# Optimization experiments

Measured on AMD Instinct MI355X. Metric: run time of the kernel, lower is better.

## Reference

```python
import jax, jax.numpy as jnp
import numpy as np
from jax import lax

B, H, S = 256, 256, 512


def setup_inputs() -> dict:
    key = jax.random.key(0)
    ks = jax.random.split(key, 7)
    sc = 1.0 / np.sqrt(H).astype(np.float32)
    tree_state = jax.random.normal(ks[0], (B, H), jnp.float32)
    seq_states = jax.random.normal(ks[1], (B, H, S), jnp.float32)
    seq_mask = jax.random.randint(ks[2], (B, S), 0, 2, jnp.int32)
    W_ih = jax.random.uniform(ks[3], (3 * H, H), jnp.float32, -sc, sc)
    W_hh = jax.random.uniform(ks[4], (3 * H, H), jnp.float32, -sc, sc)
    b_ih = jax.random.uniform(ks[5], (3 * H,), jnp.float32, -sc, sc)
    b_hh = jax.random.uniform(ks[6], (3 * H,), jnp.float32, -sc, sc)
    return {"tree_state": tree_state, "seq_states": seq_states, "seq_mask": seq_mask,
            "W_ih": W_ih, "W_hh": W_hh, "b_ih": b_ih, "b_hh": b_hh}


def _gru_cell(x, h, W_ih, W_hh, b_ih, b_hh):
    # torch.nn.GRUCell math. x, h: (B, H); W_*: (3H, H); b_*: (3H,)
    gi = x @ W_ih.T + b_ih          # (B, 3H)
    gh = h @ W_hh.T + b_hh          # (B, 3H)
    i_r, i_z, i_n = jnp.split(gi, 3, axis=-1)
    h_r, h_z, h_n = jnp.split(gh, 3, axis=-1)
    r = jax.nn.sigmoid(i_r + h_r)
    z = jax.nn.sigmoid(i_z + h_z)
    n = jnp.tanh(i_n + r * h_n)
    return (1.0 - z) * n + z * h


def reference(tree_state, seq_states, seq_mask, W_ih, W_hh, b_ih, b_hh):
    # sequential recurrent scan over the seq axis of seq_states (batch, hid, seq)
    xs = jnp.transpose(seq_states, (2, 0, 1))  # (S, B, H)

    def step(h, x):
        h_new = _gru_cell(x, h, W_ih, W_hh, b_ih, b_hh)
        return h_new, h_new

    _, outs = lax.scan(step, tree_state, xs)      # (S, B, H)
    rnn_out = jnp.transpose(outs, (1, 0, 2))      # (B, S, H)
    # get_final_encoder_states: last unmasked timestep per row
    last_idx = jnp.maximum(jnp.sum(seq_mask, axis=1) - 1, 0)  # (B,)
    final = jnp.take_along_axis(rnn_out, last_idx[:, None, None], axis=1)  # (B,1,H)
    return final[:, 0, :]
```

## Files before the change

kernel.cpp:

```cpp
#include <hip/hip_runtime.h>
#include <hip/hip_bf16.h>

#define HH 256
#define SSL 512
#define G3 768

using short8 = __attribute__((ext_vector_type(8))) short;
using f32x4  = __attribute__((ext_vector_type(4))) float;

__device__ __forceinline__ unsigned short f2bf(float f) {
  unsigned int u = __float_as_uint(f);
  u += 0x7FFFu + ((u >> 16) & 1u);
  return (unsigned short)(u >> 16);
}
__device__ __forceinline__ float bf2f(unsigned short b) {
  return __uint_as_float(((unsigned int)b) << 16);
}
__device__ __forceinline__ void block_sync_lds() {
  asm volatile("s_waitcnt lgkmcnt(0)\n\ts_barrier" ::: "memory");
}

__global__ __launch_bounds__(256) void prep_pack(
    const float* __restrict__ Wih, const float* __restrict__ Whh,
    unsigned short* __restrict__ wih_bf, unsigned short* __restrict__ whh_frag)
{
  int blk = blockIdx.x;
  if (blk < 96) {
    int base = (blk * 256 + threadIdx.x) * 4;
#pragma unroll
    for (int i = 0; i < 4; i++) {
      int u = base + i;
      float a = Wih[2 * u], b = Wih[2 * u + 1];
      ((unsigned int*)wih_bf)[u] = (unsigned int)f2bf(a) | ((unsigned int)f2bf(b) << 16);
    }
  } else {
    int gid = (blk - 96) * 256 + threadIdx.x;
    int f = gid >> 6, l = gid & 63;
    int kt = f & 7, mt = (f >> 3) & 1, g = (f >> 4) % 3, w = f / 48;
    int row = g * HH + w * 32 + mt * 16 + (l & 15);
    int k0  = kt * 32 + (l >> 4) * 8;
    const float* src = Whh + (size_t)row * HH + k0;
    unsigned int o[4];
#pragma unroll
    for (int i = 0; i < 4; i++)
      o[i] = (unsigned int)f2bf(src[2 * i]) | ((unsigned int)f2bf(src[2 * i + 1]) << 16);
    *(uint4*)(whh_frag + ((size_t)f * 64 + l) * 8) = *(uint4*)o;
  }
}

__global__ __launch_bounds__(512, 4) void gi_gemm(
    const float* __restrict__ X, const unsigned short* __restrict__ Wb,
    const float* __restrict__ bih, const float* __restrict__ bhh,
    unsigned short* __restrict__ gi)
{
  __shared__ __align__(16) char smem[36864];
  unsigned short* Al = (unsigned short*)smem;
  unsigned short* Bl = (unsigned short*)(smem + 16384);
  float (*Dl)[132] = (float(*)[132])smem;

  const int tid  = threadIdx.x;
  const int lane = tid & 63;
  const int wave = tid >> 6;
  const int wm   = wave >> 2;
  const int wj   = wave & 3;
  const int n16  = lane & 15;
  const int quad = lane >> 4;

  const int mblk = blockIdx.y;
  const int b    = mblk >> 2;
  const int s0   = (mblk & 3) * 128;
  const int j0   = blockIdx.x * 128;

  f32x4 acc[4][2];
#pragma unroll
  for (int mt = 0; mt < 4; mt++)
#pragma unroll
    for (int jt = 0; jt < 2; jt++) acc[mt][jt] = f32x4{0.f, 0.f, 0.f, 0.f};

  const float* Xb = X + (size_t)b * (HH * SSL);

  float4 xa[2][2];
  uint4  wbv[2];

  auto ldA = [&](int kt, int q, float4* dst) {
    int idx = tid + 512 * q, sq = idx & 31, a = idx >> 5;
    const float* p = Xb + (size_t)(kt * 64 + 2 * a) * SSL + s0 + 4 * sq;
    dst[0] = *(const float4*)p;
    dst[1] = *(const float4*)(p + SSL);
  };
  auto ldB = [&](int kt, int q) -> uint4 {
    int cid = tid + 512 * q, j = cid >> 3, c = cid & 7;
    return *(const uint4*)(Wb + (size_t)(j0 + j) * HH + kt * 64 + c * 8);
  };

  ldA(0, 0, xa[0]); ldA(0, 1, xa[1]);
  wbv[0] = ldB(0, 0); wbv[1] = ldB(0, 1);

  for (int kt = 0; kt < 4; kt++) {
#pragma unroll
    for (int q = 0; q < 2; q++) {
      int idx = tid + 512 * q, sq = idx & 31, a = idx >> 5;
      int c = a >> 2, d = a & 3;
#pragma unroll
      for (int r = 0; r < 4; r++) {
        int s = 4 * sq + r;
        int sw = (s + (s >> 3)) & 7;
        unsigned int u =
            (unsigned int)f2bf(((const float*)&xa[q][0])[r]) |
            ((unsigned int)f2bf(((const float*)&xa[q][1])[r]) << 16);
        *(unsigned int*)(Al + s * 64 + ((c ^ sw) * 8) + d * 2) = u;
      }
    }
#pragma unroll
    for (int p = 0; p < 2; p++) {
      int cid = tid + 512 * p, j = cid >> 3, c = cid & 7;
      int sw = (j + (j >> 3)) & 7;
      *(uint4*)(Bl + j * 64 + ((c ^ sw) * 8)) = wbv[p];
    }
    __syncthreads();
    if (kt < 3) {
      ldA(kt + 1, 0, xa[0]); ldA(kt + 1, 1, xa[1]);
      wbv[0] = ldB(kt + 1, 0); wbv[1] = ldB(kt + 1, 1);
    }
#pragma unroll
    for (int kk = 0; kk < 2; kk++) {
      short8 af[4], bfr[2];
#pragma unroll
      for (int mt = 0; mt < 4; mt++) {
        int s = wm * 64 + mt * 16 + n16;
        int sw = (s + (s >> 3)) & 7;
        af[mt] = *(const short8*)(Al + s * 64 + (((kk * 4 + quad) ^ sw) * 8));
      }
#pragma unroll
      for (int jt = 0; jt < 2; jt++) {
        int j = wj * 32 + jt * 16 + n16;
        int sw = (j + (j >> 3)) & 7;
        bfr[jt] = *(const short8*)(Bl + j * 64 + (((kk * 4 + quad) ^ sw) * 8));
      }
#pragma unroll
      for (int mt = 0; mt < 4; mt++)
#pragma unroll
        for (int jt = 0; jt < 2; jt++)
          acc[mt][jt] = __builtin_amdgcn_mfma_f32_16x16x32_bf16(af[mt], bfr[jt], acc[mt][jt], 0, 0, 0);
    }
    __syncthreads();
  }

  float bias[2];
  {
    int jg0 = j0 + wj * 32 + 0 * 16 + n16;
    int jg1 = j0 + wj * 32 + 1 * 16 + n16;
    bias[0] = bih[jg0] + (jg0 < 2 * HH ? bhh[jg0] : 0.f);
    bias[1] = bih[jg1] + (jg1 < 2 * HH ? bhh[jg1] : 0.f);
  }

  for (int c = 0; c < 2; c++) {
    __syncthreads();
    if (wm == c) {
#pragma unroll
      for (int mt = 0; mt < 4; mt++)
#pragma unroll
        for (int jt = 0; jt < 2; jt++)
#pragma unroll
          for (int r = 0; r < 4; r++)
            Dl[mt * 16 + quad * 4 + r][wj * 32 + jt * 16 + n16] = acc[mt][jt][r] + bias[jt];
    }
    __syncthreads();
#pragma unroll
    for (int i = 0; i < 2; i++) {
      int ml = (tid >> 4) + 32 * i;
      int jj = (tid & 15) * 8;
      float4 p0 = *(const float4*)&Dl[ml][jj];
      float4 p1 = *(const float4*)&Dl[ml][jj + 4];
      short8 st;
      st[0] = (short)f2bf(p0.x); st[1] = (short)f2bf(p0.y);
      st[2] = (short)f2bf(p0.z); st[3] = (short)f2bf(p0.w);
      st[4] = (short)f2bf(p1.x); st[5] = (short)f2bf(p1.y);
      st[6] = (short)f2bf(p1.z); st[7] = (short)f2bf(p1.w);
      int sgl = s0 + c * 64 + ml;
      *(short8*)(gi + ((size_t)b * SSL + sgl) * G3 + j0 + jj) = st;
    }
  }
}

__global__ __launch_bounds__(512, 2) void gru_scan(
    const float* __restrict__ tree, const int* __restrict__ mask,
    const unsigned short* __restrict__ wfrag, const float* __restrict__ bhh,
    const unsigned short* __restrict__ gi, float* __restrict__ out)
{
  __shared__ __align__(16) unsigned char lds[82432];
  unsigned short* wlds = (unsigned short*)lds;
  unsigned short (*hfrag)[8][4][4][8] =
      (unsigned short(*)[8][4][4][8])(lds + 65536);
  float* preF = (float*)(lds + 69632);
  int*   lsum = (int*)(lds + 82304);

  const int tid  = threadIdx.x;
  const int lane = tid & 63;
  const int w    = tid >> 6;
  const int n16  = lane & 15;
  const int quad = lane >> 4;
  const int brow0 = blockIdx.x * 4;
  const int bb = tid >> 7;
  const int jj = (tid & 127) * 2;

  if (tid < 4) lsum[tid] = 0;
#pragma unroll
  for (int i = 0; i < 8; i++) {
    int cid = tid + 512 * i;
    int l = cid & 63, rest = cid >> 6;
    int ktp = rest & 3, mtp = (rest >> 2) & 1, wp = rest >> 3;
    int F = ((wp * 3 + 2) * 2 + mtp) * 8 + (4 + ktp);
    uint4 v = *(const uint4*)(wfrag + ((size_t)F * 64 + l) * 8);
    *(uint4*)(wlds + (((size_t)((wp * 2 + mtp) * 4 + ktp)) * 64 + l) * 8) = v;
  }
  __syncthreads();
  {
    const int* mp = mask + (size_t)(brow0 + bb) * SSL + (tid & 127) * 4;
    atomicAdd(&lsum[bb], mp[0] + mp[1] + mp[2] + mp[3]);
  }

  short8 aw[2][2][8];
#pragma unroll
  for (int g = 0; g < 2; g++)
#pragma unroll
    for (int mt = 0; mt < 2; mt++)
#pragma unroll
      for (int kt = 0; kt < 8; kt++) {
        int F = ((w * 3 + g) * 2 + mt) * 8 + kt;
        aw[g][mt][kt] = *(const short8*)(wfrag + ((size_t)F * 64 + lane) * 8);
      }
  short8 awC[2][4];
#pragma unroll
  for (int mt = 0; mt < 2; mt++)
#pragma unroll
    for (int kt = 0; kt < 4; kt++) {
      int F = ((w * 3 + 2) * 2 + mt) * 8 + kt;
      awC[mt][kt] = *(const short8*)(wfrag + ((size_t)F * 64 + lane) * 8);
    }
#pragma unroll
  for (int g = 0; g < 2; g++)
#pragma unroll
    for (int mt = 0; mt < 2; mt++)
#pragma unroll
      for (int kt = 0; kt < 8; kt++)
        asm volatile("" : "+a"(aw[g][mt][kt]));
#pragma unroll
  for (int mt = 0; mt < 2; mt++)
#pragma unroll
    for (int kt = 0; kt < 4; kt++)
      asm volatile("" : "+a"(awC[mt][kt]));

  float bhn0 = bhh[2 * HH + jj], bhn1 = bhh[2 * HH + jj + 1];

  float h0 = tree[(size_t)(brow0 + bb) * HH + jj];
  float h1 = tree[(size_t)(brow0 + bb) * HH + jj + 1];
  *(unsigned int*)&hfrag[0][jj >> 5][bb][(jj >> 3) & 3][jj & 7] =
      (unsigned int)f2bf(h0) | ((unsigned int)f2bf(h1) << 16);
  __syncthreads();
  int last = lsum[bb] - 1; if (last < 0) last = 0;

  const unsigned short* gib = gi + (size_t)(brow0 + bb) * SSL * G3;
  unsigned int giA[3], giB[3];
#pragma unroll
  for (int g = 0; g < 3; g++) giA[g] = *(const unsigned int*)(gib + (size_t)0 * G3 + g * HH + jj);
#pragma unroll
  for (int g = 0; g < 3; g++) giB[g] = *(const unsigned int*)(gib + (size_t)1 * G3 + g * HH + jj);

  auto step = [&](int t, unsigned int* gv) {
    const int cb = t & 1, nb = cb ^ 1;
    float gir0 = bf2f((unsigned short)(gv[0] & 0xFFFF)), gir1 = bf2f((unsigned short)(gv[0] >> 16));
    float giz0 = bf2f((unsigned short)(gv[1] & 0xFFFF)), giz1 = bf2f((unsigned short)(gv[1] >> 16));
    float gin0 = bf2f((unsigned short)(gv[2] & 0xFFFF)), gin1 = bf2f((unsigned short)(gv[2] >> 16));

#pragma unroll
    for (int mt = 0; mt < 2; mt++) {
      f32x4 a0 = f32x4{0.f, 0.f, 0.f, 0.f};
      f32x4 a1 = f32x4{0.f, 0.f, 0.f, 0.f};
      f32x4 a2 = f32x4{0.f, 0.f, 0.f, 0.f};
#pragma unroll
      for (int kt = 0; kt < 8; kt++) {
        short8 hb = *(const short8*)&hfrag[cb][kt][n16 & 3][quad][0];
        a0 = __builtin_amdgcn_mfma_f32_16x16x32_bf16(aw[0][mt][kt], hb, a0, 0, 0, 0);
        a1 = __builtin_amdgcn_mfma_f32_16x16x32_bf16(aw[1][mt][kt], hb, a1, 0, 0, 0);
        short8 w2 = (kt < 4) ? awC[mt][kt]
                  : *(const short8*)(wlds + (((size_t)((w * 2 + mt) * 4 + (kt - 4))) * 64 + lane) * 8);
        a2 = __builtin_amdgcn_mfma_f32_16x16x32_bf16(w2, hb, a2, 0, 0, 0);
      }
      if (n16 < 4) {
        *(f32x4*)(preF + 0 * 1056 + n16 * 264 + w * 32 + mt * 16 + quad * 4) = a0;
        *(f32x4*)(preF + 1 * 1056 + n16 * 264 + w * 32 + mt * 16 + quad * 4) = a1;
        *(f32x4*)(preF + 2 * 1056 + n16 * 264 + w * 32 + mt * 16 + quad * 4) = a2;
      }
    }
    int tn = (t + 2 < SSL) ? t + 2 : SSL - 1;
    gv[0] = *(const unsigned int*)(gib + (size_t)tn * G3 + 0 * HH + jj);
    gv[1] = *(const unsigned int*)(gib + (size_t)tn * G3 + 1 * HH + jj);
    gv[2] = *(const unsigned int*)(gib + (size_t)tn * G3 + 2 * HH + jj);
    block_sync_lds();

    float2 pr = *(const float2*)(preF + 0 * 1056 + bb * 264 + jj);
    float2 pz = *(const float2*)(preF + 1 * 1056 + bb * 264 + jj);
    float2 pn = *(const float2*)(preF + 2 * 1056 + bb * 264 + jj);
    float hr0 = pr.x + gir0, hr1 = pr.y + gir1;
    float hz0 = pz.x + giz0, hz1 = pz.y + giz1;
    float hn0 = pn.x + bhn0, hn1 = pn.y + bhn1;
    float r0 = __builtin_amdgcn_rcpf(1.f + __expf(-hr0));
    float r1 = __builtin_amdgcn_rcpf(1.f + __expf(-hr1));
    float z0 = __builtin_amdgcn_rcpf(1.f + __expf(-hz0));
    float z1 = __builtin_amdgcn_rcpf(1.f + __expf(-hz1));
    float a0 = gin0 + r0 * hn0, a1 = gin1 + r1 * hn1;
    float nn0 = 1.f - 2.f * __builtin_amdgcn_rcpf(__expf(2.f * a0) + 1.f);
    float nn1 = 1.f - 2.f * __builtin_amdgcn_rcpf(__expf(2.f * a1) + 1.f);
    float hN0 = nn0 + z0 * (h0 - nn0);
    float hN1 = nn1 + z1 * (h1 - nn1);
    h0 = hN0; h1 = hN1;
    *(unsigned int*)&hfrag[nb][jj >> 5][bb][(jj >> 3) & 3][jj & 7] =
        (unsigned int)f2bf(hN0) | ((unsigned int)f2bf(hN1) << 16);
    if (t == last) {
      out[(size_t)(brow0 + bb) * HH + jj] = hN0;
      out[(size_t)(brow0 + bb) * HH + jj + 1] = hN1;
    }
    block_sync_lds();
  };

  for (int t = 0; t < SSL; t += 2) {
    step(t, giA);
    step(t + 1, giB);
  }
}

extern "C" void kernel_launch(void* const* d_in, const int* in_sizes, int n_in,
                              void* d_out, int out_size, void* d_ws, size_t ws_size,
                              hipStream_t stream) {
  const float* tree = (const float*)d_in[0];
  const float* seq  = (const float*)d_in[1];
  const int*   mask = (const int*)d_in[2];
  const float* Wih  = (const float*)d_in[3];
  const float* Whh  = (const float*)d_in[4];
  const float* bih  = (const float*)d_in[5];
  const float* bhh  = (const float*)d_in[6];
  float* out = (float*)d_out;

  unsigned short* gi      = (unsigned short*)d_ws;
  unsigned short* wih_bf  = (unsigned short*)((char*)d_ws + 201326592);
  unsigned short* whh_frag= (unsigned short*)((char*)d_ws + 201719808);

  prep_pack<<<192, 256, 0, stream>>>(Wih, Whh, wih_bf, whh_frag);
  gi_gemm<<<dim3(6, 1024), 512, 0, stream>>>(seq, wih_bf, bih, bhh, gi);
  gru_scan<<<64, 512, 0, stream>>>(tree, mask, whh_frag, bhh, gi, out);
}
```

Measured before the change: 1.007 ms.

## Halve scan block to 4 waves, keep all W_hh fragments in registers

The recurrent scan kernel moves from 8 waves to 4 waves per block, each wave owning 64 gate rows. The whole W_hh slice now lives in AGPRs and VGPRs instead of partly in LDS. The h-state buffer gets a padded layout, and each thread handles 4 hidden elements with wider gi loads. The aim is to cut per-step LDS weight traffic and barrier cost across fewer waves, in exchange for more MFMAs per wave and heavy register pressure at one block per CU.

```diff
diff --git a/kernel.cpp b/kernel.cpp
--- a/kernel.cpp
+++ b/kernel.cpp
@@ -36,8 +36,8 @@
   } else {
     int gid = (blk - 96) * 256 + threadIdx.x;
     int f = gid >> 6, l = gid & 63;
-    int kt = f & 7, mt = (f >> 3) & 1, g = (f >> 4) % 3, w = f / 48;
-    int row = g * HH + w * 32 + mt * 16 + (l & 15);
+    int kt = f & 7, mt = (f >> 3) & 3, g = (f >> 5) % 3, w = f / 96;
+    int row = g * HH + w * 64 + mt * 16 + (l & 15);
     int k0  = kt * 32 + (l >> 4) * 8;
     const float* src = Whh + (size_t)row * HH + k0;
     unsigned int o[4];
@@ -183,17 +183,14 @@
   }
 }
 
-__global__ __launch_bounds__(512, 2) void gru_scan(
+__global__ __launch_bounds__(256, 1) void gru_scan(
     const float* __restrict__ tree, const int* __restrict__ mask,
     const unsigned short* __restrict__ wfrag, const float* __restrict__ bhh,
     const unsigned short* __restrict__ gi, float* __restrict__ out)
 {
-  __shared__ __align__(16) unsigned char lds[82432];
-  unsigned short* wlds = (unsigned short*)lds;
-  unsigned short (*hfrag)[8][4][4][8] =
-      (unsigned short(*)[8][4][4][8])(lds + 65536);
-  float* preF = (float*)(lds + 69632);
-  int*   lsum = (int*)(lds + 82304);
+  __shared__ __align__(16) unsigned short hbuf[2][1088];
+  __shared__ __align__(16) float preF[3][4][264];
+  __shared__ int lsum[4];
 
   const int tid  = threadIdx.x;
   const int lane = tid & 63;
@@ -201,132 +198,145 @@
   const int n16  = lane & 15;
   const int quad = lane >> 4;
   const int brow0 = blockIdx.x * 4;
-  const int bb = tid >> 7;
-  const int jj = (tid & 127) * 2;
+  const int jj   = lane * 4;
 
   if (tid < 4) lsum[tid] = 0;
-#pragma unroll
-  for (int i = 0; i < 8; i++) {
-    int cid = tid + 512 * i;
-    int l = cid & 63, rest = cid >> 6;
-    int ktp = rest & 3, mtp = (rest >> 2) & 1, wp = rest >> 3;
-    int F = ((wp * 3 + 2) * 2 + mtp) * 8 + (4 + ktp);
-    uint4 v = *(const uint4*)(wfrag + ((size_t)F * 64 + l) * 8);
-    *(uint4*)(wlds + (((size_t)((wp * 2 + mtp) * 4 + ktp)) * 64 + l) * 8) = v;
+
+  f32x4 h4 = *(const f32x4*)(tree + (size_t)(brow0 + w) * HH + jj);
+  float h0 = h4[0], h1 = h4[1], h2 = h4[2], h3 = h4[3];
+  const int wslot = ((jj >> 5) * 17 + w * 4 + ((jj >> 3) & 3)) * 8 + (jj & 7);
+  {
+    unsigned long long u =
+        (unsigned long long)((unsigned)f2bf(h0) | ((unsigned)f2bf(h1) << 16)) |
+        ((unsigned long long)((unsigned)f2bf(h2) | ((unsigned)f2bf(h3) << 16)) << 32);
+    *(unsigned long long*)&hbuf[0][wslot] = u;
   }
   __syncthreads();
   {
-    const int* mp = mask + (size_t)(brow0 + bb) * SSL + (tid & 127) * 4;
-    atomicAdd(&lsum[bb], mp[0] + mp[1] + mp[2] + mp[3]);
-  }
-
-  short8 aw[2][2][8];
+    const int* mp = mask + (size_t)(brow0 + w) * SSL + lane * 8;
+    int4 a = *(const int4*)mp;
+    int4 b = *(const int4*)(mp + 4);
+    atomicAdd(&lsum[w], a.x + a.y + a.z + a.w + b.x + b.y + b.z + b.w);
+  }
+
+  short8 awA[2][4][8];
+  short8 awV[4][8];
 #pragma unroll
   for (int g = 0; g < 2; g++)
 #pragma unroll
-    for (int mt = 0; mt < 2; mt++)
+    for (int mt = 0; mt < 4; mt++)
 #pragma unroll
       for (int kt = 0; kt < 8; kt++) {
-        int F = ((w * 3 + g) * 2 + mt) * 8 + kt;
-        aw[g][mt][kt] = *(const short8*)(wfrag + ((size_t)F * 64 + lane) * 8);
-      }
-  short8 awC[2][4];
-#pragma unroll
-  for (int mt = 0; mt < 2; mt++)
-#pragma unroll
-    for (int kt = 0; kt < 4; kt++) {
-      int F = ((w * 3 + 2) * 2 + mt) * 8 + kt;
-      awC[mt][kt] = *(const short8*)(wfrag + ((size_t)F * 64 + lane) * 8);
+        int F = ((w * 3 + g) * 4 + mt) * 8 + kt;
+        awA[g][mt][kt] = *(const short8*)(wfrag + ((size_t)F * 64 + lane) * 8);
+      }
+#pragma unroll
+  for (int mt = 0; mt < 4; mt++)
+#pragma unroll
+    for (int kt = 0; kt < 8; kt++) {
+      int F = ((w * 3 + 2) * 4 + mt) * 8 + kt;
+      awV[mt][kt] = *(const short8*)(wfrag + ((size_t)F * 64 + lane) * 8);
     }
 #pragma unroll
   for (int g = 0; g < 2; g++)
 #pragma unroll
-    for (int mt = 0; mt < 2; mt++)
+    for (int mt = 0; mt < 4; mt++)
 #pragma unroll
       for (int kt = 0; kt < 8; kt++)
-        asm volatile("" : "+a"(aw[g][mt][kt]));
-#pragma unroll
-  for (int mt = 0; mt < 2; mt++)
-#pragma unroll
-    for (int kt = 0; kt < 4; kt++)
-      asm volatile("" : "+a"(awC[mt][kt]));
-
-  float bhn0 = bhh[2 * HH + jj], bhn1 = bhh[2 * HH + jj + 1];
-
-  float h0 = tree[(size_t)(brow0 + bb) * HH + jj];
-  float h1 = tree[(size_t)(brow0 + bb) * HH + jj + 1];
-  *(unsigned int*)&hfrag[0][jj >> 5][bb][(jj >> 3) & 3][jj & 7] =
-      (unsigned int)f2bf(h0) | ((unsigned int)f2bf(h1) << 16);
+        asm volatile("" : "+a"(awA[g][mt][kt]));
+#pragma unroll
+  for (int mt = 0; mt < 4; mt++)
+#pragma unroll
+    for (int kt = 0; kt < 8; kt++)
+      asm volatile("" : "+v"(awV[mt][kt]));
+
+  f32x4 bh4 = *(const f32x4*)(bhh + 2 * HH + jj);
+
+  const unsigned short* gib = gi + (size_t)(brow0 + w) * SSL * G3 + jj;
+  unsigned long long gA[3], gB[3];
+#pragma unroll
+  for (int g = 0; g < 3; g++) gA[g] = *(const unsigned long long*)(gib + (size_t)0 * G3 + g * HH);
+#pragma unroll
+  for (int g = 0; g < 3; g++) gB[g] = *(const unsigned long long*)(gib + (size_t)1 * G3 + g * HH);
+
   __syncthreads();
-  int last = lsum[bb] - 1; if (last < 0) last = 0;
-
-  const unsigned short* gib = gi + (size_t)(brow0 + bb) * SSL * G3;
-  unsigned int giA[3], giB[3];
-#pragma unroll
-  for (int g = 0; g < 3; g++) giA[g] = *(const unsigned int*)(gib + (size_t)0 * G3 + g * HH + jj);
-#pragma unroll
-  for (int g = 0; g < 3; g++) giB[g] = *(const unsigned int*)(gib + (size_t)1 * G3 + g * HH + jj);
-
-  auto step = [&](int t, unsigned int* gv) {
+  int last = lsum[w] - 1; if (last < 0) last = 0;
+
+  auto step = [&](int t, unsigned long long* gv) {
     const int cb = t & 1, nb = cb ^ 1;
-    float gir0 = bf2f((unsigned short)(gv[0] & 0xFFFF)), gir1 = bf2f((unsigned short)(gv[0] >> 16));
-    float giz0 = bf2f((unsigned short)(gv[1] & 0xFFFF)), giz1 = bf2f((unsigned short)(gv[1] >> 16));
-    float gin0 = bf2f((unsigned short)(gv[2] & 0xFFFF)), gin1 = bf2f((unsigned short)(gv[2] >> 16));
-
-#pragma unroll
-    for (int mt = 0; mt < 2; mt++) {
-      f32x4 a0 = f32x4{0.f, 0.f, 0.f, 0.f};
-      f32x4 a1 = f32x4{0.f, 0.f, 0.f, 0.f};
-      f32x4 a2 = f32x4{0.f, 0.f, 0.f, 0.f};
+    unsigned long long g0 = gv[0], g1 = gv[1], g2 = gv[2];
+
+    const unsigned short* hp = &hbuf[cb][0] + ((n16 & 3) * 4 + quad) * 8;
+    short8 hb[8];
+#pragma unroll
+    for (int kt = 0; kt < 8; kt++)
+      hb[kt] = *(const short8*)(hp + kt * (17 * 8));
+
+    int tn = (t + 2 < SSL) ? t + 2 : SSL - 1;
+    gv[0] = *(const unsigned long long*)(gib + (size_t)tn * G3 + 0 * HH);
+    gv[1] = *(const unsigned long long*)(gib + (size_t)tn * G3 + 1 * HH);
+    gv[2] = *(const unsigned long long*)(gib + (size_t)tn * G3 + 2 * HH);
+
+#pragma unroll
+    for (int mp = 0; mp < 2; mp++) {
+      const int m0 = 2 * mp, m1 = 2 * mp + 1;
+      f32x4 ar0 = f32x4{0.f, 0.f, 0.f, 0.f}, az0 = ar0, an0 = ar0;
+      f32x4 ar1 = ar0, az1 = ar0, an1 = ar0;
 #pragma unroll
       for (int kt = 0; kt < 8; kt++) {
-        short8 hb = *(const short8*)&hfrag[cb][kt][n16 & 3][quad][0];
-        a0 = __builtin_amdgcn_mfma_f32_16x16x32_bf16(aw[0][mt][kt], hb, a0, 0, 0, 0);
-        a1 = __builtin_amdgcn_mfma_f32_16x16x32_bf16(aw[1][mt][kt], hb, a1, 0, 0, 0);
-        short8 w2 = (kt < 4) ? awC[mt][kt]
-                  : *(const short8*)(wlds + (((size_t)((w * 2 + mt) * 4 + (kt - 4))) * 64 + lane) * 8);
-        a2 = __builtin_amdgcn_mfma_f32_16x16x32_bf16(w2, hb, a2, 0, 0, 0);
+        ar0 = __builtin_amdgcn_mfma_f32_16x16x32_bf16(awA[0][m0][kt], hb[kt], ar0, 0, 0, 0);
+        ar1 = __builtin_amdgcn_mfma_f32_16x16x32_bf16(awA[0][m1][kt], hb[kt], ar1, 0, 0, 0);
+        az0 = __builtin_amdgcn_mfma_f32_16x16x32_bf16(awA[1][m0][kt], hb[kt], az0, 0, 0, 0);
+        az1 = __builtin_amdgcn_mfma_f32_16x16x32_bf16(awA[1][m1][kt], hb[kt], az1, 0, 0, 0);
+        an0 = __builtin_amdgcn_mfma_f32_16x16x32_bf16(awV[m0][kt],    hb[kt], an0, 0, 0, 0);
+        an1 = __builtin_amdgcn_mfma_f32_16x16x32_bf16(awV[m1][kt],    hb[kt], an1, 0, 0, 0);
       }
       if (n16 < 4) {
-        *(f32x4*)(preF + 0 * 1056 + n16 * 264 + w * 32 + mt * 16 + quad * 4) = a0;
-        *(f32x4*)(preF + 1 * 1056 + n16 * 264 + w * 32 + mt * 16 + quad * 4) = a1;
-        *(f32x4*)(preF + 2 * 1056 + n16 * 264 + w * 32 + mt * 16 + quad * 4) = a2;
-      }
-    }
-    int tn = (t + 2 < SSL) ? t + 2 : SSL - 1;
-    gv[0] = *(const unsigned int*)(gib + (size_t)tn * G3 + 0 * HH + jj);
-    gv[1] = *(const unsigned int*)(gib + (size_t)tn * G3 + 1 * HH + jj);
-    gv[2] = *(const unsigned int*)(gib + (size_t)tn * G3 + 2 * HH + jj);
+        int r0 = w * 64 + m0 * 16 + quad * 4;
+        int r1 = w * 64 + m1 * 16 + quad * 4;
+        *(f32x4*)&preF[0][n16][r0] = ar0;
+        *(f32x4*)&preF[0][n16][r1] = ar1;
+        *(f32x4*)&preF[1][n16][r0] = az0;
+        *(f32x4*)&preF[1][n16][r1] = az1;
+        *(f32x4*)&preF[2][n16][r0] = an0;
+        *(f32x4*)&preF[2][n16][r1] = an1;
+      }
+    }
     block_sync_lds();
 
-    float2 pr = *(const float2*)(preF + 0 * 1056 + bb * 264 + jj);
-    float2 pz = *(const float2*)(preF + 1 * 1056 + bb * 264 + jj);
-    float2 pn = *(const float2*)(preF + 2 * 1056 + bb * 264 + jj);
-    float hr0 = pr.x + gir0, hr1 = pr.y + gir1;
-    float hz0 = pz.x + giz0, hz1 = pz.y + giz1;
-    float hn0 = pn.x + bhn0, hn1 = pn.y + bhn1;
-    float r0 = __builtin_amdgcn_rcpf(1.f + __expf(-hr0));
-    float r1 = __builtin_amdgcn_rcpf(1.f + __expf(-hr1));
-    float z0 = __builtin_amdgcn_rcpf(1.f + __expf(-hz0));
-    float z1 = __builtin_amdgcn_rcpf(1.f + __expf(-hz1));
-    float a0 = gin0 + r0 * hn0, a1 = gin1 + r1 * hn1;
-    float nn0 = 1.f - 2.f * __builtin_amdgcn_rcpf(__expf(2.f * a0) + 1.f);
-    float nn1 = 1.f - 2.f * __builtin_amdgcn_rcpf(__expf(2.f * a1) + 1.f);
-    float hN0 = nn0 + z0 * (h0 - nn0);
-    float hN1 = nn1 + z1 * (h1 - nn1);
-    h0 = hN0; h1 = hN1;
-    *(unsigned int*)&hfrag[nb][jj >> 5][bb][(jj >> 3) & 3][jj & 7] =
-        (unsigned int)f2bf(hN0) | ((unsigned int)f2bf(hN1) << 16);
+    f32x4 pr = *(const f32x4*)&preF[0][w][jj];
+    f32x4 pz = *(const f32x4*)&preF[1][w][jj];
+    f32x4 pn = *(const f32x4*)&preF[2][w][jj];
+
+    float hv[4] = {h0, h1, h2, h3};
+#pragma unroll
+    for (int e = 0; e < 4; e++) {
+      float gr = bf2f((unsigned short)((g0 >> (16 * e)) & 0xFFFFull));
+      float gz = bf2f((unsigned short)((g1 >> (16 * e)) & 0xFFFFull));
+      float gn = bf2f((unsigned short)((g2 >> (16 * e)) & 0xFFFFull));
+      float r = __builtin_amdgcn_rcpf(1.f + __expf(-(pr[e] + gr)));
+      float z = __builtin_amdgcn_rcpf(1.f + __expf(-(pz[e] + gz)));
+      float a = gn + r * (pn[e] + bh4[e]);
+      float nn = 1.f - 2.f * __builtin_amdgcn_rcpf(__expf(2.f * a) + 1.f);
+      hv[e] = nn + z * (hv[e] - nn);
+    }
+    h0 = hv[0]; h1 = hv[1]; h2 = hv[2]; h3 = hv[3];
+    {
+      unsigned long long u =
+          (unsigned long long)((unsigned)f2bf(h0) | ((unsigned)f2bf(h1) << 16)) |
+          ((unsigned long long)((unsigned)f2bf(h2) | ((unsigned)f2bf(h3) << 16)) << 32);
+      *(unsigned long long*)&hbuf[nb][wslot] = u;
+    }
     if (t == last) {
-      out[(size_t)(brow0 + bb) * HH + jj] = hN0;
-      out[(size_t)(brow0 + bb) * HH + jj + 1] = hN1;
+      f32x4 o = {h0, h1, h2, h3};
+      *(f32x4*)(out + (size_t)(brow0 + w) * HH + jj) = o;
     }
     block_sync_lds();
   };
 
   for (int t = 0; t < SSL; t += 2) {
-    step(t, giA);
-    step(t + 1, giB);
+    step(t, gA);
+    step(t + 1, gB);
   }
 }
 
@@ -348,5 +358,5 @@
 
   prep_pack<<<192, 256, 0, stream>>>(Wih, Whh, wih_bf, whh_frag);
   gi_gemm<<<dim3(6, 1024), 512, 0, stream>>>(seq, wih_bf, bih, bhh, gi);
-  gru_scan<<<64, 512, 0, stream>>>(tree, mask, whh_frag, bhh, gi, out);
-}
+  gru_scan<<<64, 256, 0, stream>>>(tree, mask, whh_frag, bhh, gi, out);
+}
```

New measurement: 1.038 ms. 1.03x slower.
